# Optimization experiments

Hardware: AMD Instinct MI355X
Metric: run time of the kernel (lower is better)

Reference implementation:

```python
import jax, jax.numpy as jnp
import numpy as np
from jax.scipy.ndimage import map_coordinates

H, W = 200, 200            # detector pixels
SDD = 1020.0               # source-to-detector distance (mm)
DELX, DELY = 2.0, 2.0      # detector pixel pitch (mm)
VOL = 256                  # volume side (voxels, 1mm spacing)
N_SAMPLES = 500


def setup_inputs() -> dict:
    key = jax.random.key(0)
    volume = jax.random.uniform(key, (VOL, VOL, VOL), dtype=jnp.float32)
    # intrinsics: K maps camera-space ray dirs to pixels; k_inv is its inverse
    cx, cy = (W - 1) / 2.0, (H - 1) / 2.0
    K = np.array([[SDD / DELX, 0.0, cx],
                  [0.0, SDD / DELY, cy],
                  [0.0, 0.0, 1.0]], dtype=np.float32)
    k_inv = jnp.asarray(np.linalg.inv(K))[None]           # [1,3,3]
    sdd = jnp.array([SDD], dtype=jnp.float32)             # [1]
    # extrinsic pose: camera (source) placed at world z=-300mm, axes aligned
    rt = np.eye(4, dtype=np.float32)
    rt[2, 3] = -300.0
    rt_inv = jnp.asarray(rt)[None]                        # [1,4,4]
    # world (mm) -> voxel index: volume centered at origin, 1mm spacing
    aff = np.eye(4, dtype=np.float32)
    aff[:3, 3] = (VOL - 1) / 2.0
    affine_inv = jnp.asarray(aff)                         # [4,4]
    return {"volume": volume, "k_inv": k_inv, "rt_inv": rt_inv,
            "sdd": sdd, "affine_inv": affine_inv, "n_samples": N_SAMPLES}


def reference(volume, k_inv, rt_inv, sdd, affine_inv, n_samples):
    dt = volume.dtype
    B = k_inv.shape[0]
    # detector pixel grid -> camera-space target points on the detector plane
    uu, vv = jnp.meshgrid(jnp.arange(W, dtype=dt), jnp.arange(H, dtype=dt), indexing="xy")
    pix = jnp.stack([uu, vv, jnp.ones_like(uu)], axis=-1).reshape(-1, 3)   # [N,3]
    tgt_cam = jnp.einsum("bij,nj->bni", k_inv, pix) * sdd[:, None, None]  # [B,N,3]
    # world-space source and targets
    R, t = rt_inv[:, :3, :3], rt_inv[:, :3, 3]
    src = t                                                               # [B,3] camera origin
    tgt = jnp.einsum("bij,bnj->bni", R, tgt_cam) + t[:, None, :]          # [B,N,3]
    # sample points uniformly along each ray (align_corners=True endpoints)
    ts = jnp.linspace(0.0, 1.0, n_samples, dtype=dt)                      # [S]
    ray = tgt - src[:, None, :]                                           # [B,N,3]
    pts = src[:, None, None, :] + ts[None, None, :, None] * ray[:, :, None, :]  # [B,N,S,3]
    # world -> voxel coordinates
    vox = jnp.einsum("ij,bnsj->bnsi", affine_inv[:3, :3], pts) + affine_inv[:3, 3]
    # trilinear interpolation of the volume at every sample point
    samp = map_coordinates(
        volume,
        [vox[..., 0].ravel(), vox[..., 1].ravel(), vox[..., 2].ravel()],
        order=1, mode="constant", cval=0.0,
    ).reshape(B, H * W, n_samples)
    # integrate along the ray (rectangle rule with per-ray step length)
    step = jnp.linalg.norm(ray, axis=-1) / (n_samples - 1)                # [B,N]
    img = (samp.sum(axis=-1) * step).reshape(B, H, W)
    return img
```

## Files before the change

### kernel.cpp

```cpp
#include <hip/hip_runtime.h>

#define IMG_H 200
#define IMG_W 200
#define VOLD  256
#define KPH   16

__global__ __launch_bounds__(256) void drr_kernel(
    const float* __restrict__ vol,
    const float* __restrict__ kinv,
    const float* __restrict__ rt,
    const float* __restrict__ sddp,
    const float* __restrict__ aff,
    const int*   __restrict__ nsp,
    float*       __restrict__ out)
{
    const int tid   = blockIdx.x * blockDim.x + threadIdx.x;
    const int p     = tid / KPH;
    const int phase = tid & (KPH - 1);
    if (p >= IMG_H * IMG_W) return;

    const int   N     = nsp[0];
    const float sdd   = sddp[0];
    const float invN1 = 1.0f / (float)(N - 1);

    const float u = (float)(p % IMG_W);
    const float v = (float)(p / IMG_W);

    const float tcx = (kinv[0]*u + kinv[1]*v + kinv[2]) * sdd;
    const float tcy = (kinv[3]*u + kinv[4]*v + kinv[5]) * sdd;
    const float tcz = (kinv[6]*u + kinv[7]*v + kinv[8]) * sdd;

    const float rx = rt[0]*tcx + rt[1]*tcy + rt[2]*tcz;
    const float ry = rt[4]*tcx + rt[5]*tcy + rt[6]*tcz;
    const float rz = rt[8]*tcx + rt[9]*tcy + rt[10]*tcz;
    const float sx = rt[3], sy = rt[7], sz = rt[11];

    const float bx = aff[0]*sx + aff[1]*sy + aff[2]*sz  + aff[3];
    const float by = aff[4]*sx + aff[5]*sy + aff[6]*sz  + aff[7];
    const float bz = aff[8]*sx + aff[9]*sy + aff[10]*sz + aff[11];
    const float dx = aff[0]*rx + aff[1]*ry + aff[2]*rz;
    const float dy = aff[4]*ry ? (aff[4]*rx + aff[5]*ry + aff[6]*rz)
                               : (aff[4]*rx + aff[5]*ry + aff[6]*rz);
    const float dy2 = aff[4]*rx + aff[5]*ry + aff[6]*rz;
    const float dz = aff[8]*rx + aff[9]*ry + aff[10]*rz;
    const float DY = dy2; (void)dy;

    float t0 = 0.0f, t1 = 1.0f;
    {
        const float lo = -1.0f, hi = (float)VOLD;
        const float bs[3] = {bx, by, bz};
        const float ds[3] = {dx, DY, dz};
        #pragma unroll
        for (int d = 0; d < 3; ++d) {
            const float b  = bs[d];
            const float dd = ds[d];
            if (fabsf(dd) > 1e-20f) {
                const float ta = (lo - b) / dd;
                const float tb = (hi - b) / dd;
                t0 = fmaxf(t0, fminf(ta, tb));
                t1 = fminf(t1, fmaxf(ta, tb));
            } else if (b <= lo || b >= hi) {
                t0 = 1.0f; t1 = -1.0f;
            }
        }
    }
    int s_lo = 0, s_hi = -1;
    if (t0 <= t1) {
        s_lo = (int)floorf(t0 * (float)(N - 1)) - 1;
        s_hi = (int)ceilf (t1 * (float)(N - 1)) + 1;
        s_lo = max(s_lo, 0);
        s_hi = min(s_hi, N - 1);
    }

    float acc = 0.0f;
    #pragma unroll 2
    for (int s = s_lo + phase; s <= s_hi; s += KPH) {
        const float t = (float)s * invN1;
        const float x = fmaf(t, dx, bx);
        const float y = fmaf(t, DY, by);
        const float z = fmaf(t, dz, bz);
        const float fx = floorf(x), fy = floorf(y), fz = floorf(z);
        const int ix = (int)fx, iy = (int)fy, iz = (int)fz;
        const float wx = x - fx, wy = y - fy, wz = z - fz;

        float c000, c001, c010, c011, c100, c101, c110, c111;
        if ((unsigned)ix < 255u && (unsigned)iy < 255u && (unsigned)iz < 255u) {
            const float* pb = vol + ((ix << 16) + (iy << 8) + iz);
            c000 = pb[0];         c001 = pb[1];
            c010 = pb[256];       c011 = pb[257];
            c100 = pb[65536];     c101 = pb[65537];
            c110 = pb[65536+256]; c111 = pb[65536+257];
        } else {
            const bool x0 = (unsigned)ix       < 256u;
            const bool x1 = (unsigned)(ix + 1) < 256u;
            const bool y0 = (unsigned)iy       < 256u;
            const bool y1 = (unsigned)(iy + 1) < 256u;
            const bool z0 = (unsigned)iz       < 256u;
            const bool z1 = (unsigned)(iz + 1) < 256u;
            const int bx0 = ix << 16, bx1 = (ix + 1) << 16;
            const int by0 = iy << 8,  by1 = (iy + 1) << 8;
            c000 = (x0 && y0 && z0) ? vol[bx0 + by0 + iz]     : 0.0f;
            c001 = (x0 && y0 && z1) ? vol[bx0 + by0 + iz + 1] : 0.0f;
            c010 = (x0 && y1 && z0) ? vol[bx0 + by1 + iz]     : 0.0f;
            c011 = (x0 && y1 && z1) ? vol[bx0 + by1 + iz + 1] : 0.0f;
            c100 = (x1 && y0 && z0) ? vol[bx1 + by0 + iz]     : 0.0f;
            c101 = (x1 && y0 && z1) ? vol[bx1 + by0 + iz + 1] : 0.0f;
            c110 = (x1 && y1 && z0) ? vol[bx1 + by1 + iz]     : 0.0f;
            c111 = (x1 && y1 && z1) ? vol[bx1 + by1 + iz + 1] : 0.0f;
        }

        const float c00 = fmaf(wz, c001 - c000, c000);
        const float c01 = fmaf(wz, c011 - c010, c010);
        const float c10 = fmaf(wz, c101 - c100, c100);
        const float c11 = fmaf(wz, c111 - c110, c110);
        const float c0  = fmaf(wy, c01 - c00, c00);
        const float c1  = fmaf(wy, c11 - c10, c10);
        acc += fmaf(wx, c1 - c0, c0);
    }

    acc += __shfl_down(acc, 8, KPH);
    acc += __shfl_down(acc, 4, KPH);
    acc += __shfl_down(acc, 2, KPH);
    acc += __shfl_down(acc, 1, KPH);

    if (phase == 0) {
        const float step = sqrtf(rx*rx + ry*ry + rz*rz) * invN1;
        out[p] = acc * step;
    }
}

extern "C" void kernel_launch(void* const* d_in, const int* in_sizes, int n_in,
                              void* d_out, int out_size, void* d_ws, size_t ws_size,
                              hipStream_t stream) {
    const float* vol  = (const float*)d_in[0];
    const float* kinv = (const float*)d_in[1];
    const float* rt   = (const float*)d_in[2];
    const float* sdd  = (const float*)d_in[3];
    const float* aff  = (const float*)d_in[4];
    const int*   nsp  = (const int*)d_in[5];
    float* out = (float*)d_out;

    const long long threads = (long long)IMG_H * IMG_W * KPH;
    dim3 block(256);
    dim3 grid((unsigned)((threads + 255) / 256));
    drr_kernel<<<grid, block, 0, stream>>>(vol, kinv, rt, sdd, aff, nsp, out);
}
```

Before: 112.5 us.

## Halve threads per ray, remap blocks across XCDs, unroll sampling loop deeper

Drops threads per ray from 16 to 8, so each block covers 32 pixels and each thread takes more samples. Block IDs are remapped so consecutive pixel tiles land on the same XCD, which is meant to improve L2 reuse of neighbouring voxels. The sampling loop is unrolled 4 instead of 2, and the slab-clip divides are replaced with reciprocal multiplies, with the sample-range margin widened from 1 to 2 to guard against the less exact reciprocal. With half as many threads in flight, each thread runs a longer serial loop, which may reduce the latency hiding available for the gathers.

Result: no change. 111.4 us (-0.9%).

```diff
diff --git a/kernel.cpp b/kernel.cpp
--- a/kernel.cpp
+++ b/kernel.cpp
@@ -3,7 +3,11 @@
 #define IMG_H 200
 #define IMG_W 200
 #define VOLD  256
-#define KPH   16
+#define KPH   8
+#define PPB   (256 / KPH)
+#define NPIX  (IMG_H * IMG_W)
+#define NBLK  (NPIX / PPB)
+#define NXCD  8
 
 __global__ __launch_bounds__(256) void drr_kernel(
     const float* __restrict__ vol,
@@ -14,10 +18,19 @@
     const int*   __restrict__ nsp,
     float*       __restrict__ out)
 {
-    const int tid   = blockIdx.x * blockDim.x + threadIdx.x;
-    const int p     = tid / KPH;
-    const int phase = tid & (KPH - 1);
-    if (p >= IMG_H * IMG_W) return;
+    int b = blockIdx.x;
+    {
+        const int q = NBLK / NXCD;
+        const int r = NBLK % NXCD;
+        const int xcd = b % NXCD;
+        const int idx = b / NXCD;
+        b = (xcd < r) ? xcd * (q + 1) + idx
+                      : r * (q + 1) + (xcd - r) * q + idx;
+    }
+
+    const int p     = b * PPB + ((int)threadIdx.x >> 3);
+    const int phase = (int)threadIdx.x & (KPH - 1);
+    if (p >= NPIX) return;
 
     const int   N     = nsp[0];
     const float sdd   = sddp[0];
@@ -39,45 +52,43 @@
     const float by = aff[4]*sx + aff[5]*sy + aff[6]*sz  + aff[7];
     const float bz = aff[8]*sx + aff[9]*sy + aff[10]*sz + aff[11];
     const float dx = aff[0]*rx + aff[1]*ry + aff[2]*rz;
-    const float dy = aff[4]*ry ? (aff[4]*rx + aff[5]*ry + aff[6]*rz)
-                               : (aff[4]*rx + aff[5]*ry + aff[6]*rz);
-    const float dy2 = aff[4]*rx + aff[5]*ry + aff[6]*rz;
+    const float dy = aff[4]*rx + aff[5]*ry + aff[6]*rz;
     const float dz = aff[8]*rx + aff[9]*ry + aff[10]*rz;
-    const float DY = dy2; (void)dy;
 
     float t0 = 0.0f, t1 = 1.0f;
     {
         const float lo = -1.0f, hi = (float)VOLD;
         const float bs[3] = {bx, by, bz};
-        const float ds[3] = {dx, DY, dz};
+        const float ds[3] = {dx, dy, dz};
         #pragma unroll
         for (int d = 0; d < 3; ++d) {
-            const float b  = bs[d];
+            const float bq = bs[d];
             const float dd = ds[d];
             if (fabsf(dd) > 1e-20f) {
-                const float ta = (lo - b) / dd;
-                const float tb = (hi - b) / dd;
+                const float rdd = __frcp_rn(dd);
+                const float ta = (lo - bq) * rdd;
+                const float tb = (hi - bq) * rdd;
                 t0 = fmaxf(t0, fminf(ta, tb));
                 t1 = fminf(t1, fmaxf(ta, tb));
-            } else if (b <= lo || b >= hi) {
+            } else if (bq <= lo || bq >= hi) {
                 t0 = 1.0f; t1 = -1.0f;
             }
         }
     }
     int s_lo = 0, s_hi = -1;
     if (t0 <= t1) {
-        s_lo = (int)floorf(t0 * (float)(N - 1)) - 1;
-        s_hi = (int)ceilf (t1 * (float)(N - 1)) + 1;
+        s_lo = (int)floorf(t0 * (float)(N - 1)) - 2;
+        s_hi = (int)ceilf (t1 * (float)(N - 1)) + 2;
         s_lo = max(s_lo, 0);
         s_hi = min(s_hi, N - 1);
     }
 
     float acc = 0.0f;
-    #pragma unroll 2
+    #pragma unroll 4
     for (int s = s_lo + phase; s <= s_hi; s += KPH) {
         const float t = (float)s * invN1;
         const float x = fmaf(t, dx, bx);
-        const float y = fmaf(t, DY, by);
+        const float y = fmaf(t, dy, by);
         const float z = fmaf(t, dz, bz);
         const float fx = floorf(x), fy = floorf(y), fz = floorf(z);
         const int ix = (int)fx, iy = (int)fy, iz = (int)fz;
@@ -118,7 +129,6 @@
         acc += fmaf(wx, c1 - c0, c0);
     }
 
-    acc += __shfl_down(acc, 8, KPH);
     acc += __shfl_down(acc, 4, KPH);
     acc += __shfl_down(acc, 2, KPH);
     acc += __shfl_down(acc, 1, KPH);
@@ -140,8 +150,7 @@
     const int*   nsp  = (const int*)d_in[5];
     float* out = (float*)d_out;
 
-    const long long threads = (long long)IMG_H * IMG_W * KPH;
     dim3 block(256);
-    dim3 grid((unsigned)((threads + 255) / 256));
+    dim3 grid(NBLK);
     drr_kernel<<<grid, block, 0, stream>>>(vol, kinv, rt, sdd, aff, nsp, out);
 }
```
